# Kernel tuning notes

Measured on AMD Instinct MI355X. Metric: run time of the kernel, lower is better.

Reference implementation:

```python
import jax, jax.numpy as jnp
import numpy as np
import math

HEAD_DIM = 128
N_HEADS = 32
HIDDEN = 4096
ROPE_THETA = 10000.0
NEG = -100000.0


def _rope_cos_sin(pos):
    # pos: [B, L] int -> cos, sin: [B, L, HEAD_DIM]
    inv_freq = 1.0 / (ROPE_THETA ** (jnp.arange(0, HEAD_DIM, 2, dtype=jnp.float32) / HEAD_DIM))
    freqs = pos.astype(jnp.float32)[..., None] * inv_freq  # [B, L, HEAD_DIM//2]
    emb = jnp.concatenate([freqs, freqs], axis=-1)
    return jnp.cos(emb), jnp.sin(emb)


def _rotate_half(x):
    x1, x2 = x[..., : HEAD_DIM // 2], x[..., HEAD_DIM // 2 :]
    return jnp.concatenate([-x2, x1], axis=-1)


def _apply_rope(h, cos, sin):
    # h: [B, H, L, D], cos/sin: [B, L, D] -> unsqueeze head dim
    return h * cos[:, None] + _rotate_half(h) * sin[:, None]


def setup_inputs() -> dict:
    key = jax.random.key(0)
    ks = jax.random.split(key, 8)
    B, Q, K = 2, 1024, 2048
    inp = {
        "hidden_states": jax.random.normal(ks[0], (B, Q, HIDDEN), jnp.float32),
        "key_value_states": jax.random.normal(ks[1], (B, K, HIDDEN), jnp.float32),
        "Wq": jax.random.normal(ks[2], (HIDDEN, HIDDEN), jnp.float32) * 0.02,
        "Wk": jax.random.normal(ks[3], (HIDDEN, HIDDEN), jnp.float32) * 0.02,
        "Wv": jax.random.normal(ks[4], (HIDDEN, HIDDEN), jnp.float32) * 0.02,
        "Wo": jax.random.normal(ks[5], (HIDDEN, HIDDEN), jnp.float32) * 0.02,
        "position_ids": jnp.arange(B * Q, dtype=jnp.int32).reshape(B, Q),
        "text_position_ids": jnp.arange(B * K, dtype=jnp.int32).reshape(B, K),
        "simul_mask_idx": jnp.sort(jax.random.randint(ks[6], (B, Q), 0, K, jnp.int32), axis=-1),
        "window_size": jax.random.randint(ks[7], (B, Q), 0, 512, jnp.int32),
    }
    return inp


def reference(hidden_states, key_value_states, Wq, Wk, Wv, Wo,
              position_ids, text_position_ids, simul_mask_idx, window_size):
    B, Qlen, _ = hidden_states.shape
    Klen = key_value_states.shape[1]

    q = jnp.einsum('bqh,hd->bqd', hidden_states, Wq.T).reshape(B, Qlen, N_HEADS, HEAD_DIM).transpose(0, 2, 1, 3)
    k = jnp.einsum('bkh,hd->bkd', key_value_states, Wk.T).reshape(B, Klen, N_HEADS, HEAD_DIM).transpose(0, 2, 1, 3)
    v = jnp.einsum('bkh,hd->bkd', key_value_states, Wv.T).reshape(B, Klen, N_HEADS, HEAD_DIM).transpose(0, 2, 1, 3)

    cos, sin = _rope_cos_sin(position_ids)
    q = _apply_rope(q, cos, sin)
    t_cos, t_sin = _rope_cos_sin(text_position_ids)
    k = _apply_rope(k, t_cos, t_sin)

    scores = jnp.einsum('bhqd,bhkd->bhqk', q, k) / math.sqrt(HEAD_DIM)

    # simul windowed mask: key j visible for query i iff clamp(idx-w,0) <= j < idx
    idx = simul_mask_idx[:, None, :, None]          # [B,1,Q,1]
    w = window_size[:, None, :, None]               # [B,1,Q,1]
    tmp = jnp.arange(Klen, dtype=jnp.int32)         # [K]
    mask = (jnp.clip(idx - w, 0) <= tmp) & (tmp < idx)  # [B,1,Q,K]
    scores = jnp.where(mask, scores, NEG)

    probs = jax.nn.softmax(scores.astype(jnp.float32), axis=-1).astype(q.dtype)
    attn = jnp.einsum('bhqk,bhkd->bhqd', probs, v)
    attn = attn.transpose(0, 2, 1, 3).reshape(B, Qlen, HIDDEN)
    out = jnp.einsum('bqh,hd->bqd', attn, Wo.T)
    return out
```

## Files before the change

### kernel.cpp

```cpp
#include <hip/hip_runtime.h>
#include <stdint.h>

#define BATCH 2
#define QLEN 1024
#define KLEN 2048
#define NH 32
#define HD 128
#define HID 4096

typedef short bf16x8 __attribute__((ext_vector_type(8)));
typedef float f32x4 __attribute__((ext_vector_type(4)));
typedef unsigned short u16;

typedef const __attribute__((address_space(1))) void gvoid;
typedef __attribute__((address_space(3))) void lvoid;

__device__ __forceinline__ u16 f2bf(float f) {
  union { float f; uint32_t u; } x; x.f = f;
  uint32_t r = x.u + 0x7fffu + ((x.u >> 16) & 1u);
  return (u16)(r >> 16);
}
__device__ __forceinline__ float bf2f(u16 h) {
  union { uint32_t u; float f; } x; x.u = ((uint32_t)h) << 16;
  return x.f;
}
__device__ __forceinline__ f32x4 mfma16(bf16x8 a, bf16x8 b, f32x4 c) {
  return __builtin_amdgcn_mfma_f32_16x16x32_bf16(a, b, c, 0, 0, 0);
}
__device__ __forceinline__ void glds16(const u16* src, char* dst) {
  __builtin_amdgcn_global_load_lds((gvoid*)src, (lvoid*)dst, 16, 0, 0);
}

__global__ __launch_bounds__(256) void cvt_kernel(const float* __restrict__ in,
                                                  u16* __restrict__ out, int n) {
  int i = (blockIdx.x * 256 + threadIdx.x) * 8;
  if (i >= n) return;
  const float4* p = (const float4*)(in + i);
  float4 a = p[0], b = p[1];
  union { u16 h[8]; bf16x8 v; } u;
  u.h[0] = f2bf(a.x); u.h[1] = f2bf(a.y); u.h[2] = f2bf(a.z); u.h[3] = f2bf(a.w);
  u.h[4] = f2bf(b.x); u.h[5] = f2bf(b.y); u.h[6] = f2bf(b.z); u.h[7] = f2bf(b.w);
  *(bf16x8*)(out + i) = u.v;
}

#define RD_A(CB, ks, mf) (*(const bf16x8*)(lds + (CB) + (ks) * 16384 + (mf) * 1024 + rA))
#define RD_B(CB, ks, nf) (*(const bf16x8*)(lds + 65536 + (CB) + (ks) * 16384 + (nf) * 1024 + rB))

#define TILE256(CB, NB, K0N)                                                     \
  {                                                                              \
    bf16x8 af[4], bfr[4], af2[4];                                                \
    _Pragma("unroll") for (int x = 0; x < 4; x++) af[x] = RD_A(CB, 0, x);        \
    _Pragma("unroll") for (int x = 0; x < 4; x++) bfr[x] = RD_B(CB, 0, x);       \
    glds16(As0 + (K0N), dA + (NB));                                              \
    glds16(As1 + (K0N), dA + (NB) + 8192);                                       \
    __builtin_amdgcn_s_barrier();                                                \
    asm volatile("s_waitcnt lgkmcnt(0)" ::: "memory");                           \
    __builtin_amdgcn_sched_barrier(0);                                           \
    __builtin_amdgcn_s_setprio(1);                                               \
    _Pragma("unroll") for (int mf = 0; mf < 4; mf++)                             \
      _Pragma("unroll") for (int nf = 0; nf < 4; nf++)                           \
        acc[mf][nf] = mfma16(af[mf], bfr[nf], acc[mf][nf]);                      \
    __builtin_amdgcn_s_setprio(0);                                               \
    __builtin_amdgcn_s_barrier();                                                \
    _Pragma("unroll") for (int x = 0; x < 4; x++) af2[x] = RD_A(CB, 0, 4 + x);   \
    glds16(Bs0 + (K0N), dB + (NB));                                              \
    glds16(Bs1 + (K0N), dB + (NB) + 8192);                                       \
    asm volatile("s_waitcnt vmcnt(4)" ::: "memory");                             \
    __builtin_amdgcn_s_barrier();                                                \
    asm volatile("s_waitcnt lgkmcnt(0)" ::: "memory");                           \
    __builtin_amdgcn_sched_barrier(0);                                           \
    __builtin_amdgcn_s_setprio(1);                                               \
    _Pragma("unroll") for (int mf = 0; mf < 4; mf++)                             \
      _Pragma("unroll") for (int nf = 0; nf < 4; nf++)                           \
        acc[4 + mf][nf] = mfma16(af2[mf], bfr[nf], acc[4 + mf][nf]);             \
    __builtin_amdgcn_s_setprio(0);                                               \
    __builtin_amdgcn_s_barrier();                                                \
    _Pragma("unroll") for (int x = 0; x < 4; x++) af[x] = RD_A(CB, 1, x);        \
    _Pragma("unroll") for (int x = 0; x < 4; x++) bfr[x] = RD_B(CB, 1, x);       \
    glds16(As0 + (K0N) + 32, dA + (NB) + 16384);                                 \
    glds16(As1 + (K0N) + 32, dA + (NB) + 16384 + 8192);                          \
    __builtin_amdgcn_s_barrier();                                                \
    asm volatile("s_waitcnt lgkmcnt(0)" ::: "memory");                           \
    __builtin_amdgcn_sched_barrier(0);                                           \
    __builtin_amdgcn_s_setprio(1);                                               \
    _Pragma("unroll") for (int mf = 0; mf < 4; mf++)                             \
      _Pragma("unroll") for (int nf = 0; nf < 4; nf++)                           \
        acc[mf][nf] = mfma16(af[mf], bfr[nf], acc[mf][nf]);                      \
    __builtin_amdgcn_s_setprio(0);                                               \
    __builtin_amdgcn_s_barrier();                                                \
    _Pragma("unroll") for (int x = 0; x < 4; x++) af2[x] = RD_A(CB, 1, 4 + x);   \
    glds16(Bs0 + (K0N) + 32, dB + (NB) + 16384);                                 \
    glds16(Bs1 + (K0N) + 32, dB + (NB) + 16384 + 8192);                          \
    asm volatile("s_waitcnt vmcnt(4)" ::: "memory");                             \
    __builtin_amdgcn_s_barrier();                                                \
    asm volatile("s_waitcnt lgkmcnt(0)" ::: "memory");                           \
    __builtin_amdgcn_sched_barrier(0);                                           \
    __builtin_amdgcn_s_setprio(1);                                               \
    _Pragma("unroll") for (int mf = 0; mf < 4; mf++)                             \
      _Pragma("unroll") for (int nf = 0; nf < 4; nf++)                           \
        acc[4 + mf][nf] = mfma16(af2[mf], bfr[nf], acc[4 + mf][nf]);             \
    __builtin_amdgcn_s_setprio(0);                                               \
    __builtin_amdgcn_s_barrier();                                                \
  }

template <int EPI>
__global__ __launch_bounds__(512, 2) void gemm256(const u16* __restrict__ A,
                                                  const u16* __restrict__ Bw,
                                                  void* __restrict__ Cout,
                                                  int M, int N, int K) {
  (void)M;
  __shared__ alignas(16) char lds[131072];
  const int tid = threadIdx.x;
  const int lane = tid & 63, wv = tid >> 6;
  const int wvm = wv >> 2, wvn = wv & 3;
  const int g = lane >> 4, l16 = lane & 15;
  const int m0 = blockIdx.y * 256, n0 = blockIdx.x * 256;

  const int srow = tid >> 2;
  const int sg = (tid & 3) ^ (srow & 3);
  const u16* As0 = A + (size_t)(m0 + srow) * K + sg * 8;
  const u16* As1 = A + (size_t)(m0 + 128 + srow) * K + sg * 8;
  const u16* Bs0 = Bw + (size_t)(n0 + srow) * K + sg * 8;
  const u16* Bs1 = Bw + (size_t)(n0 + 128 + srow) * K + sg * 8;
  char* dA = lds + tid * 16;
  char* dB = lds + 65536 + tid * 16;

  const int rsw = (g ^ (l16 & 3)) << 4;
  const int rA = (wvm * 128 + l16) * 64 + rsw;
  const int rB = (wvn * 64 + l16) * 64 + rsw;

  f32x4 acc[8][4];
#pragma unroll
  for (int mf = 0; mf < 8; mf++)
#pragma unroll
    for (int nf = 0; nf < 4; nf++) acc[mf][nf] = (f32x4){0.f, 0.f, 0.f, 0.f};

  glds16(As0, dA);
  glds16(As1, dA + 8192);
  glds16(Bs0, dB);
  glds16(Bs1, dB + 8192);
  glds16(As0 + 32, dA + 16384);
  glds16(As1 + 32, dA + 16384 + 8192);
  glds16(Bs0 + 32, dB + 16384);
  glds16(Bs1 + 32, dB + 16384 + 8192);
  asm volatile("s_waitcnt vmcnt(4)" ::: "memory");
  __builtin_amdgcn_s_barrier();

  const int NT = K >> 6;
  for (int t = 0; t < NT; t += 2) {
    const int kA = (t + 1) * 64;
    TILE256(0, 32768, kA)
    const int kB = (((t + 2) < NT) ? (t + 2) : 0) * 64;
    TILE256(32768, 0, kB)
  }

  if (EPI == 2) {
    u16* C = (u16*)Cout;
#pragma unroll
    for (int mf = 0; mf < 8; mf++) {
      int rowb = m0 + wvm * 128 + mf * 16 + g * 4;
#pragma unroll
      for (int nf = 0; nf < 4; nf++) {
        int col = n0 + wvn * 64 + nf * 16 + l16;
#pragma unroll
        for (int j = 0; j < 4; j++)
          C[(size_t)(rowb + j) * N + col] = f2bf(acc[mf][nf][j]);
      }
    }
  } else {
    u16* C = (u16*)Cout;
#pragma unroll
    for (int mf = 0; mf < 8; mf++) {
      int rowb = m0 + wvm * 128 + mf * 16 + g * 4;
      int bb = rowb >> 11, tt = rowb & 2047;
#pragma unroll
      for (int nf = 0; nf < 4; nf++) {
        int col = n0 + wvn * 64 + nf * 16 + l16;
        uint64_t pk = (uint64_t)f2bf(acc[mf][nf][0]) |
                      ((uint64_t)f2bf(acc[mf][nf][1]) << 16) |
                      ((uint64_t)f2bf(acc[mf][nf][2]) << 32) |
                      ((uint64_t)f2bf(acc[mf][nf][3]) << 48);
        *(uint64_t*)(C + ((size_t)(bb * 4096 + col)) * 2048 + tt) = pk;
      }
    }
  }
}

#define BM 128
#define BN 128
#define BKK 32

template <int EPI>
__global__ __launch_bounds__(256, 2) void gemm_bt(const u16* __restrict__ A,
                                                  const u16* __restrict__ Bw,
                                                  void* __restrict__ Cout,
                                                  int M, int N, int K) {
  __shared__ u16 As[BM * BKK];
  __shared__ u16 Bs[BN * BKK];
  const int tid = threadIdx.x;
  const int lane = tid & 63, wv = tid >> 6;
  const int m0 = blockIdx.y * BM, n0 = blockIdx.x * BN;
  const int g = lane >> 4, l16 = lane & 15;
  const int wm = (wv >> 1) * 64, wn = (wv & 1) * 64;

  const int o0 = wv * 2048 + lane * 16;
  const int row0 = o0 >> 6;
  const int cb0 = o0 & 63;
  const uint8_t* ag0 = (const uint8_t*)A + ((size_t)(m0 + row0) * K) * 2 + cb0;
  const uint8_t* ag1 = ag0 + (size_t)16 * K * 2;
  const uint8_t* bg0 = (const uint8_t*)Bw + ((size_t)(n0 + row0) * K) * 2 + cb0;
  const uint8_t* bg1 = bg0 + (size_t)16 * K * 2;
  char* aL0 = (char*)As + wv * 2048;
  char* aL1 = aL0 + 1024;
  char* bL0 = (char*)Bs + wv * 2048;
  char* bL1 = bL0 + 1024;

  f32x4 acc[4][4];
#pragma unroll
  for (int mf = 0; mf < 4; mf++)
#pragma unroll
    for (int nf = 0; nf < 4; nf++) acc[mf][nf] = (f32x4){0.f, 0.f, 0.f, 0.f};

  for (int k0 = 0; k0 < K; k0 += BKK) {
    __builtin_amdgcn_global_load_lds((gvoid*)ag0, (lvoid*)aL0, 16, 0, 0);
    __builtin_amdgcn_global_load_lds((gvoid*)ag1, (lvoid*)aL1, 16, 0, 0);
    __builtin_amdgcn_global_load_lds((gvoid*)bg0, (lvoid*)bL0, 16, 0, 0);
    __builtin_amdgcn_global_load_lds((gvoid*)bg1, (lvoid*)bL1, 16, 0, 0);
    ag0 += 64; ag1 += 64; bg0 += 64; bg1 += 64;
    __syncthreads();
    bf16x8 af[4], bfr[4];
#pragma unroll
    for (int mf = 0; mf < 4; mf++)
      af[mf] = *(const bf16x8*)((const char*)As + (wm + mf * 16 + l16) * 64 + g * 16);
#pragma unroll
    for (int nf = 0; nf < 4; nf++)
      bfr[nf] = *(const bf16x8*)((const char*)Bs + (wn + nf * 16 + l16) * 64 + g * 16);
#pragma unroll
    for (int mf = 0; mf < 4; mf++)
#pragma unroll
      for (int nf = 0; nf < 4; nf++)
        acc[mf][nf] = mfma16(af[mf], bfr[nf], acc[mf][nf]);
    __syncthreads();
  }

  if (EPI == 0) {
    float* C = (float*)Cout;
#pragma unroll
    for (int mf = 0; mf < 4; mf++) {
      int rowb = m0 + wm + mf * 16 + g * 4;
#pragma unroll
      for (int nf = 0; nf < 4; nf++) {
        int col = n0 + wn + nf * 16 + l16;
#pragma unroll
        for (int j = 0; j < 4; j++)
          C[(size_t)(rowb + j) * N + col] = acc[mf][nf][j];
      }
    }
  } else {
    u16* C = (u16*)Cout;
#pragma unroll
    for (int mf = 0; mf < 4; mf++) {
      int rowb = m0 + wm + mf * 16 + g * 4;
#pragma unroll
      for (int nf = 0; nf < 4; nf++) {
        int col = n0 + wn + nf * 16 + l16;
#pragma unroll
        for (int j = 0; j < 4; j++)
          C[(size_t)(rowb + j) * N + col] = f2bf(acc[mf][nf][j]);
      }
    }
  }
}

__global__ __launch_bounds__(256) void rope_kernel(const u16* __restrict__ x,
                                                   const int* __restrict__ pos,
                                                   u16* __restrict__ out,
                                                   int rowsPerB) {
  int row = blockIdx.x;
  int b = row / rowsPerB, r = row - b * rowsPerB;
  float p = (float)pos[row];
  int t = threadIdx.x;
  int h = t >> 3, i0 = (t & 7) * 8;
  const u16* xr = x + (size_t)row * HID + h * HD;
  bf16x8 lov = *(const bf16x8*)(xr + i0);
  bf16x8 hiv = *(const bf16x8*)(xr + 64 + i0);
  union { u16 h[8]; bf16x8 v; } olo, ohi;
#pragma unroll
  for (int j = 0; j < 8; j++) {
    float lo = bf2f((u16)lov[j]);
    float hi = bf2f((u16)hiv[j]);
    float f = exp2f(-(float)(i0 + j) * (13.287712379549449f / 64.0f));
    float ang = p * f;
    float s, c;
    sincosf(ang, &s, &c);
    olo.h[j] = f2bf(lo * c - hi * s);
    ohi.h[j] = f2bf(hi * c + lo * s);
  }
  u16* ob = out + ((size_t)((b * NH + h) * rowsPerB) + r) * HD;
  *(bf16x8*)(ob + i0) = olo.v;
  *(bf16x8*)(ob + 64 + i0) = ohi.v;
}

__global__ __launch_bounds__(256) void vmean_kernel(const u16* __restrict__ vt,
                                                    float* __restrict__ vm) {
  int row = blockIdx.x * 4 + (threadIdx.x >> 6);
  int lane = threadIdx.x & 63;
  const u16* p = vt + (size_t)row * KLEN;
  float s = 0.f;
#pragma unroll
  for (int it = 0; it < 4; it++) {
    bf16x8 v = *(const bf16x8*)(p + it * 512 + lane * 8);
#pragma unroll
    for (int j = 0; j < 8; j++) s += bf2f((u16)v[j]);
  }
  for (int off = 32; off; off >>= 1) s += __shfl_xor(s, off);
  if (lane == 0) vm[row] = s * (1.0f / (float)KLEN);
}

__global__ __launch_bounds__(256, 2) void attn_kernel(
    const u16* __restrict__ qb, const u16* __restrict__ kb,
    const u16* __restrict__ vt, const float* __restrict__ vm,
    const int* __restrict__ idxA, const int* __restrict__ wA,
    u16* __restrict__ aout) {
  __shared__ u16 Ks[32][136];
  __shared__ u16 Vs[128][40];
  __shared__ u16 Ps[4][16][40];
  __shared__ int sS[64], sE[64], sRange[2];

  const int tid = threadIdx.x, lane = tid & 63, wv = tid >> 6;
  const int g = lane >> 4, l16 = lane & 15;
  const int blk = blockIdx.x;
  const int qt = blk & 15, bh = blk >> 4, b = bh >> 5, h = bh & 31;
  const int q0 = qt * 64;
  const float SCALE = 0.08838834764831845f;

  if (tid < 64) {
    int e = idxA[b * QLEN + q0 + tid];
    int w = wA[b * QLEN + q0 + tid];
    int s = e - w;
    if (s < 0) s = 0;
    sS[tid] = s;
    sE[tid] = e;
  }
  __syncthreads();
  if (wv == 0) {
    int s_ = sS[lane], e_ = sE[lane];
    int mn = (e_ > s_) ? s_ : 0x7fffffff;
    int mx = (e_ > s_) ? e_ : 0;
    for (int off = 32; off; off >>= 1) {
      mn = min(mn, __shfl_xor(mn, off));
      mx = max(mx, __shfl_xor(mx, off));
    }
    if (lane == 0) { sRange[0] = mn; sRange[1] = mx; }
  }
  __syncthreads();
  const int klo = sRange[0], khi = sRange[1];

  int rs[4], re[4];
#pragma unroll
  for (int r = 0; r < 4; r++) {
    rs[r] = sS[wv * 16 + g * 4 + r];
    re[r] = sE[wv * 16 + g * 4 + r];
  }

  bf16x8 qf[4];
  {
    const u16* qp = qb + ((size_t)(bh * QLEN + q0 + wv * 16 + l16)) * HD + g * 8;
#pragma unroll
    for (int s4 = 0; s4 < 4; s4++) qf[s4] = *(const bf16x8*)(qp + s4 * 32);
  }

  f32x4 acc[8];
#pragma unroll
  for (int db = 0; db < 8; db++) acc[db] = (f32x4){0.f, 0.f, 0.f, 0.f};
  float mrow[4] = {-1e30f, -1e30f, -1e30f, -1e30f};
  float lsum[4] = {0.f, 0.f, 0.f, 0.f};

  if (klo < khi) {
    for (int t0 = (klo & ~31); t0 < khi; t0 += 32) {
      {
        int idx = tid * 8;
        int kr = idx >> 7, kc = idx & 127;
        *(bf16x8*)(&Ks[kr][kc]) =
            *(const bf16x8*)(kb + ((size_t)(bh * KLEN + t0 + kr)) * HD + kc);
        int kr2 = kr + 16;
        *(bf16x8*)(&Ks[kr2][kc]) =
            *(const bf16x8*)(kb + ((size_t)(bh * KLEN + t0 + kr2)) * HD + kc);
        int vr = idx >> 5, vc = idx & 31;
        *(bf16x8*)(&Vs[vr][vc]) =
            *(const bf16x8*)(vt + ((size_t)(bh * HD + vr)) * KLEN + t0 + vc);
        int vr2 = vr + 64;
        *(bf16x8*)(&Vs[vr2][vc]) =
            *(const bf16x8*)(vt + ((size_t)(bh * HD + vr2)) * KLEN + t0 + vc);
      }
      __syncthreads();

      f32x4 sc0 = (f32x4){0.f, 0.f, 0.f, 0.f};
      f32x4 sc1 = (f32x4){0.f, 0.f, 0.f, 0.f};
#pragma unroll
      for (int s4 = 0; s4 < 4; s4++) {
        bf16x8 k0 = *(const bf16x8*)(&Ks[l16][s4 * 32 + g * 8]);
        bf16x8 k1 = *(const bf16x8*)(&Ks[16 + l16][s4 * 32 + g * 8]);
        sc0 = mfma16(qf[s4], k0, sc0);
        sc1 = mfma16(qf[s4], k1, sc1);
      }

      float resc[4];
#pragma unroll
      for (int r = 0; r < 4; r++) {
        float v0 = sc0[r] * SCALE, v1 = sc1[r] * SCALE;
        int t_0 = t0 + l16, t_1 = t0 + 16 + l16;
        v0 = (t_0 >= rs[r] && t_0 < re[r]) ? v0 : -1e30f;
        v1 = (t_1 >= rs[r] && t_1 < re[r]) ? v1 : -1e30f;
        float mx = fmaxf(v0, v1);
        mx = fmaxf(mx, __shfl_xor(mx, 1));
        mx = fmaxf(mx, __shfl_xor(mx, 2));
        mx = fmaxf(mx, __shfl_xor(mx, 4));
        mx = fmaxf(mx, __shfl_xor(mx, 8));
        float mn = fmaxf(mrow[r], mx);
        float rc = __expf(mrow[r] - mn);
        float p0 = __expf(v0 - mn), p1 = __expf(v1 - mn);
        mrow[r] = mn;
        resc[r] = rc;
        float ps = p0 + p1;
        ps += __shfl_xor(ps, 1);
        ps += __shfl_xor(ps, 2);
        ps += __shfl_xor(ps, 4);
        ps += __shfl_xor(ps, 8);
        lsum[r] = lsum[r] * rc + ps;
        Ps[wv][g * 4 + r][l16] = f2bf(p0);
        Ps[wv][g * 4 + r][16 + l16] = f2bf(p1);
      }
#pragma unroll
      for (int db = 0; db < 8; db++) {
#pragma unroll
        for (int r = 0; r < 4; r++) acc[db][r] *= resc[r];
      }
      bf16x8 pf = *(const bf16x8*)(&Ps[wv][l16][g * 8]);
#pragma unroll
      for (int db = 0; db < 8; db++) {
        bf16x8 vf = *(const bf16x8*)(&Vs[db * 16 + l16][g * 8]);
        acc[db] = mfma16(pf, vf, acc[db]);
      }
      __syncthreads();
    }
  }

#pragma unroll
  for (int r = 0; r < 4; r++) {
    int lr = wv * 16 + g * 4 + r;
    int q = q0 + lr;
    bool empty = (re[r] <= rs[r]);
    float inv = empty ? 0.f : 1.0f / lsum[r];
    u16* orow = aout + ((size_t)(b * QLEN + q)) * HID + h * HD;
#pragma unroll
    for (int db = 0; db < 8; db++) {
      float o = empty ? vm[bh * HD + db * 16 + l16] : acc[db][r] * inv;
      orow[db * 16 + l16] = f2bf(o);
    }
  }
}

extern "C" void kernel_launch(void* const* d_in, const int* in_sizes, int n_in,
                              void* d_out, int out_size, void* d_ws, size_t ws_size,
                              hipStream_t stream) {
  (void)in_sizes; (void)n_in; (void)out_size; (void)ws_size;
  const float* hs = (const float*)d_in[0];
  const float* kvs = (const float*)d_in[1];
  const float* Wq = (const float*)d_in[2];
  const float* Wk = (const float*)d_in[3];
  const float* Wv = (const float*)d_in[4];
  const float* Wo = (const float*)d_in[5];
  const int* pos = (const int*)d_in[6];
  const int* tpos = (const int*)d_in[7];
  const int* sidx = (const int*)d_in[8];
  const int* wsz = (const int*)d_in[9];
  float* out = (float*)d_out;

  char* ws = (char*)d_ws;
  size_t off = 0;
  auto alloc = [&](size_t bytes) -> void* {
    void* p = ws + off;
    off += (bytes + 255) & ~(size_t)255;
    return p;
  };
  const size_t WN = (size_t)HID * HID;
  const size_t NQ = (size_t)BATCH * QLEN * HID;
  const size_t NK = (size_t)BATCH * KLEN * HID;

  u16* wbuf = (u16*)alloc(WN * 2);
  u16* hid_b = (u16*)alloc(NQ * 2);
  u16* kv_b = (u16*)alloc(NK * 2);
  u16* sc_b = (u16*)alloc(NK * 2);
  u16* q_b = (u16*)alloc(NQ * 2);
  u16* k_b = (u16*)alloc(NK * 2);
  u16* vt_b = (u16*)alloc(NK * 2);
  float* vmean = (float*)alloc((size_t)BATCH * NH * HD * 4);

  cvt_kernel<<<(int)(NQ / 2048), 256, 0, stream>>>(hs, hid_b, (int)NQ);
  cvt_kernel<<<(int)(NK / 2048), 256, 0, stream>>>(kvs, kv_b, (int)NK);

  cvt_kernel<<<(int)(WN / 2048), 256, 0, stream>>>(Wq, wbuf, (int)WN);
  gemm_bt<2><<<dim3(HID / 128, BATCH * QLEN / 128), 256, 0, stream>>>(
      hid_b, wbuf, sc_b, BATCH * QLEN, HID, HID);
  rope_kernel<<<BATCH * QLEN, 256, 0, stream>>>(sc_b, pos, q_b, QLEN);

  cvt_kernel<<<(int)(WN / 2048), 256, 0, stream>>>(Wk, wbuf, (int)WN);
  gemm256<2><<<dim3(HID / 256, BATCH * KLEN / 256), 512, 0, stream>>>(
      kv_b, wbuf, sc_b, BATCH * KLEN, HID, HID);
  rope_kernel<<<BATCH * KLEN, 256, 0, stream>>>(sc_b, tpos, k_b, KLEN);

  cvt_kernel<<<(int)(WN / 2048), 256, 0, stream>>>(Wv, wbuf, (int)WN);
  gemm256<1><<<dim3(HID / 256, BATCH * KLEN / 256), 512, 0, stream>>>(
      kv_b, wbuf, vt_b, BATCH * KLEN, HID, HID);
  vmean_kernel<<<BATCH * NH * HD / 4, 256, 0, stream>>>(vt_b, vmean);

  attn_kernel<<<BATCH * NH * (QLEN / 64), 256, 0, stream>>>(
      q_b, k_b, vt_b, vmean, sidx, wsz, sc_b);

  cvt_kernel<<<(int)(WN / 2048), 256, 0, stream>>>(Wo, wbuf, (int)WN);
  gemm_bt<0><<<dim3(HID / 128, BATCH * QLEN / 128), 256, 0, stream>>>(
      sc_b, wbuf, out, BATCH * QLEN, HID, HID);
}
```

Baseline: 619.1 us.

## Route Q and output projections through 256-tile GEMM and adjust LDS swizzle

The Q projection and output projection now run on the 256x256-tile, 512-thread pipelined GEMM instead of the simpler 128x128 single-buffered kernel. That GEMM gains an fp32 epilogue for the output projection, and the old kernel is deleted. The LDS XOR swizzle now keys on (row>>1)&3 instead of row&3, both where tiles are stored and where fragments are read, to cut bank conflicts. With M=2048 the bigger tiles launch only 128 blocks, which may underfill the GPU's compute units.

```diff
diff --git a/kernel.cpp b/kernel.cpp
--- a/kernel.cpp
+++ b/kernel.cpp
@@ -117,7 +117,7 @@
   const int m0 = blockIdx.y * 256, n0 = blockIdx.x * 256;
 
   const int srow = tid >> 2;
-  const int sg = (tid & 3) ^ (srow & 3);
+  const int sg = (tid & 3) ^ ((srow >> 1) & 3);
   const u16* As0 = A + (size_t)(m0 + srow) * K + sg * 8;
   const u16* As1 = A + (size_t)(m0 + 128 + srow) * K + sg * 8;
   const u16* Bs0 = Bw + (size_t)(n0 + srow) * K + sg * 8;
@@ -125,7 +125,7 @@
   char* dA = lds + tid * 16;
   char* dB = lds + 65536 + tid * 16;
 
-  const int rsw = (g ^ (l16 & 3)) << 4;
+  const int rsw = (g ^ ((l16 >> 1) & 3)) << 4;
   const int rA = (wvm * 128 + l16) * 64 + rsw;
   const int rB = (wvn * 64 + l16) * 64 + rsw;
 
@@ -154,7 +154,20 @@
     TILE256(32768, 0, kB)
   }
 
-  if (EPI == 2) {
+  if (EPI == 0) {
+    float* C = (float*)Cout;
+#pragma unroll
+    for (int mf = 0; mf < 8; mf++) {
+      int rowb = m0 + wvm * 128 + mf * 16 + g * 4;
+#pragma unroll
+      for (int nf = 0; nf < 4; nf++) {
+        int col = n0 + wvn * 64 + nf * 16 + l16;
+#pragma unroll
+        for (int j = 0; j < 4; j++)
+          C[(size_t)(rowb + j) * N + col] = acc[mf][nf][j];
+      }
+    }
+  } else if (EPI == 2) {
     u16* C = (u16*)Cout;
 #pragma unroll
     for (int mf = 0; mf < 8; mf++) {
@@ -181,92 +194,6 @@
                       ((uint64_t)f2bf(acc[mf][nf][2]) << 32) |
                       ((uint64_t)f2bf(acc[mf][nf][3]) << 48);
         *(uint64_t*)(C + ((size_t)(bb * 4096 + col)) * 2048 + tt) = pk;
-      }
-    }
-  }
-}
-
-#define BM 128
-#define BN 128
-#define BKK 32
-
-template <int EPI>
-__global__ __launch_bounds__(256, 2) void gemm_bt(const u16* __restrict__ A,
-                                                  const u16* __restrict__ Bw,
-                                                  void* __restrict__ Cout,
-                                                  int M, int N, int K) {
-  __shared__ u16 As[BM * BKK];
-  __shared__ u16 Bs[BN * BKK];
-  const int tid = threadIdx.x;
-  const int lane = tid & 63, wv = tid >> 6;
-  const int m0 = blockIdx.y * BM, n0 = blockIdx.x * BN;
-  const int g = lane >> 4, l16 = lane & 15;
-  const int wm = (wv >> 1) * 64, wn = (wv & 1) * 64;
-
-  const int o0 = wv * 2048 + lane * 16;
-  const int row0 = o0 >> 6;
-  const int cb0 = o0 & 63;
-  const uint8_t* ag0 = (const uint8_t*)A + ((size_t)(m0 + row0) * K) * 2 + cb0;
-  const uint8_t* ag1 = ag0 + (size_t)16 * K * 2;
-  const uint8_t* bg0 = (const uint8_t*)Bw + ((size_t)(n0 + row0) * K) * 2 + cb0;
-  const uint8_t* bg1 = bg0 + (size_t)16 * K * 2;
-  char* aL0 = (char*)As + wv * 2048;
-  char* aL1 = aL0 + 1024;
-  char* bL0 = (char*)Bs + wv * 2048;
-  char* bL1 = bL0 + 1024;
-
-  f32x4 acc[4][4];
-#pragma unroll
-  for (int mf = 0; mf < 4; mf++)
-#pragma unroll
-    for (int nf = 0; nf < 4; nf++) acc[mf][nf] = (f32x4){0.f, 0.f, 0.f, 0.f};
-
-  for (int k0 = 0; k0 < K; k0 += BKK) {
-    __builtin_amdgcn_global_load_lds((gvoid*)ag0, (lvoid*)aL0, 16, 0, 0);
-    __builtin_amdgcn_global_load_lds((gvoid*)ag1, (lvoid*)aL1, 16, 0, 0);
-    __builtin_amdgcn_global_load_lds((gvoid*)bg0, (lvoid*)bL0, 16, 0, 0);
-    __builtin_amdgcn_global_load_lds((gvoid*)bg1, (lvoid*)bL1, 16, 0, 0);
-    ag0 += 64; ag1 += 64; bg0 += 64; bg1 += 64;
-    __syncthreads();
-    bf16x8 af[4], bfr[4];
-#pragma unroll
-    for (int mf = 0; mf < 4; mf++)
-      af[mf] = *(const bf16x8*)((const char*)As + (wm + mf * 16 + l16) * 64 + g * 16);
-#pragma unroll
-    for (int nf = 0; nf < 4; nf++)
-      bfr[nf] = *(const bf16x8*)((const char*)Bs + (wn + nf * 16 + l16) * 64 + g * 16);
-#pragma unroll
-    for (int mf = 0; mf < 4; mf++)
-#pragma unroll
-      for (int nf = 0; nf < 4; nf++)
-        acc[mf][nf] = mfma16(af[mf], bfr[nf], acc[mf][nf]);
-    __syncthreads();
-  }
-
-  if (EPI == 0) {
-    float* C = (float*)Cout;
-#pragma unroll
-    for (int mf = 0; mf < 4; mf++) {
-      int rowb = m0 + wm + mf * 16 + g * 4;
-#pragma unroll
-      for (int nf = 0; nf < 4; nf++) {
-        int col = n0 + wn + nf * 16 + l16;
-#pragma unroll
-        for (int j = 0; j < 4; j++)
-          C[(size_t)(rowb + j) * N + col] = acc[mf][nf][j];
-      }
-    }
-  } else {
-    u16* C = (u16*)Cout;
-#pragma unroll
-    for (int mf = 0; mf < 4; mf++) {
-      int rowb = m0 + wm + mf * 16 + g * 4;
-#pragma unroll
-      for (int nf = 0; nf < 4; nf++) {
-        int col = n0 + wn + nf * 16 + l16;
-#pragma unroll
-        for (int j = 0; j < 4; j++)
-          C[(size_t)(rowb + j) * N + col] = f2bf(acc[mf][nf][j]);
       }
     }
   }
@@ -501,7 +428,7 @@
   cvt_kernel<<<(int)(NK / 2048), 256, 0, stream>>>(kvs, kv_b, (int)NK);
 
   cvt_kernel<<<(int)(WN / 2048), 256, 0, stream>>>(Wq, wbuf, (int)WN);
-  gemm_bt<2><<<dim3(HID / 128, BATCH * QLEN / 128), 256, 0, stream>>>(
+  gemm256<2><<<dim3(HID / 256, BATCH * QLEN / 256), 512, 0, stream>>>(
       hid_b, wbuf, sc_b, BATCH * QLEN, HID, HID);
   rope_kernel<<<BATCH * QLEN, 256, 0, stream>>>(sc_b, pos, q_b, QLEN);
 
@@ -519,6 +446,6 @@
       q_b, k_b, vt_b, vmean, sidx, wsz, sc_b);
 
   cvt_kernel<<<(int)(WN / 2048), 256, 0, stream>>>(Wo, wbuf, (int)WN);
-  gemm_bt<0><<<dim3(HID / 128, BATCH * QLEN / 128), 256, 0, stream>>>(
+  gemm256<0><<<dim3(HID / 256, BATCH * QLEN / 256), 512, 0, stream>>>(
       sc_b, wbuf, out, BATCH * QLEN, HID, HID);
 }
```

Result: no change. 621.6 us (+0.4%).
